# Optimization experiments

Hardware: AMD Instinct MI355X
Metric: run time of the kernel (lower is better)

## Reference

```python
import jax, jax.numpy as jnp
import numpy as np

N_ITERS = 5
STRICT_MAXIMA_BONUS = 10.0
MAX_SUBPIXEL_SHIFT = 0.6
DILATION_RADIUS = 1
EPS = 1e-7


def _dense_solve(x):
    """Per-voxel 3x3x3 quadratic-fit solve (Cramer's rule) on interior voxels.

    Returns full-size (zero-padded) sx, sy, ss, g.s, solved arrays.
    Axis convention: s = depth/scale (D), y = height (H), x = width (W).
    """
    c  = x[:, :, 1:-1, 1:-1, 1:-1]
    xp = x[:, :, 1:-1, 1:-1, 2:];   xm = x[:, :, 1:-1, 1:-1, :-2]
    yp = x[:, :, 1:-1, 2:, 1:-1];   ym = x[:, :, 1:-1, :-2, 1:-1]
    sp = x[:, :, 2:, 1:-1, 1:-1];   sm = x[:, :, :-2, 1:-1, 1:-1]
    xpyp = x[:, :, 1:-1, 2:, 2:];   xmyp = x[:, :, 1:-1, 2:, :-2]
    xpym = x[:, :, 1:-1, :-2, 2:];  xmym = x[:, :, 1:-1, :-2, :-2]
    xpsp = x[:, :, 2:, 1:-1, 2:];   xmsp = x[:, :, 2:, 1:-1, :-2]
    xpsm = x[:, :, :-2, 1:-1, 2:];  xmsm = x[:, :, :-2, 1:-1, :-2]
    ypsp = x[:, :, 2:, 2:, 1:-1];   ymsp = x[:, :, 2:, :-2, 1:-1]
    ypsm = x[:, :, :-2, 2:, 1:-1];  ymsm = x[:, :, :-2, :-2, 1:-1]
    gx = 0.5 * (xp - xm)
    gy = 0.5 * (yp - ym)
    gs = 0.5 * (sp - sm)
    dxx = xp - 2.0 * c + xm
    dyy = yp - 2.0 * c + ym
    dss = sp - 2.0 * c + sm
    dxy = 0.25 * (xpyp - xmyp - xpym + xmym)
    dxs = 0.25 * (xpsp - xmsp - xpsm + xmsm)
    dys = 0.25 * (ypsp - ymsp - ypsm + ymsm)
    cf00 = dyy * dss - dys * dys
    cf01 = dxy * dss - dys * dxs
    cf02 = dxy * dys - dyy * dxs
    det = dxx * cf00 - dxy * cf01 + dxs * cf02
    solved = jnp.abs(det) > EPS
    safe_det = jnp.where(solved, det, jnp.ones_like(det))
    r0, r1, r2 = -gx, -gy, -gs
    sx = (r0 * cf00 - dxy * (r1 * dss - dys * r2) + dxs * (r1 * dys - dyy * r2)) / safe_det
    sy = (dxx * (r1 * dss - dys * r2) - r0 * cf01 + dxs * (dxy * r2 - r1 * dxs)) / safe_det
    ss = (dxx * (dyy * r2 - r1 * dys) - dxy * (dxy * r2 - r1 * dxs) + r0 * cf02) / safe_det
    gds = gx * sx + gy * sy + gs * ss
    pad = ((0, 0), (0, 0), (1, 1), (1, 1), (1, 1))
    return (jnp.pad(sx, pad), jnp.pad(sy, pad), jnp.pad(ss, pad),
            jnp.pad(gds, pad), jnp.pad(solved, pad))


def reference(input, nms_mask):
    x = input
    B, C, D, H, W = x.shape
    dt = x.dtype
    HW = H * W
    DHW = D * HW
    r = DILATION_RADIUS

    sx_f, sy_f, ss_f, gds_f, sol_f = _dense_solve(x)
    sx_f = sx_f.reshape(-1); sy_f = sy_f.reshape(-1); ss_f = ss_f.reshape(-1)
    gds_f = gds_f.reshape(-1); sol_f = sol_f.reshape(-1)
    xf = x.reshape(-1)

    dg = jnp.arange(D, dtype=jnp.int32)[:, None, None]
    hg = jnp.arange(H, dtype=jnp.int32)[None, :, None]
    wg = jnp.arange(W, dtype=jnp.int32)[None, None, :]
    bcg = (jnp.arange(B * C, dtype=jnp.int32) * DHW).reshape(B, C, 1, 1, 1)

    zi = jnp.zeros((B, C, D, H, W), jnp.int32)
    dd, dh, dw = zi, zi, zi              # integer centre offsets (s, y, x)
    valid = nms_mask                      # only NMS maxima are tracked
    zf = jnp.zeros((B, C, D, H, W), dt)
    shift_x, shift_y, shift_s, gds_k = zf, zf, zf, zf

    for _ in range(N_ITERS):
        di = jnp.clip(dg + dd, 1, D - 2)
        hi = jnp.clip(hg + dh, 1, H - 2)
        wi = jnp.clip(wg + dw, 1, W - 2)
        flat = bcg + di * HW + hi * W + wi
        sx = sx_f[flat]; sy = sy_f[flat]; ss = ss_f[flat]
        gds = gds_f[flat]; sol = sol_f[flat]
        valid = valid & sol
        vf = valid.astype(dt)
        shift_x = sx * vf
        shift_y = sy * vf
        shift_s = ss * vf
        gds_k = gds * vf
        step_x = (jnp.sign(shift_x) * (jnp.abs(shift_x) > MAX_SUBPIXEL_SHIFT)).astype(jnp.int32)
        step_y = (jnp.sign(shift_y) * (jnp.abs(shift_y) > MAX_SUBPIXEL_SHIFT)).astype(jnp.int32)
        step_s = (jnp.sign(shift_s) * (jnp.abs(shift_s) > MAX_SUBPIXEL_SHIFT)).astype(jnp.int32)
        dw = dw + step_x; dh = dh + step_y; dd = dd + step_s
        # moving outside the dilated precompute region invalidates the keypoint
        valid = valid & (jnp.abs(dd) <= r) & (jnp.abs(dh) <= r) & (jnp.abs(dw) <= r)

    di = jnp.clip(dg + dd, 1, D - 2)
    hi = jnp.clip(hg + dh, 1, H - 2)
    wi = jnp.clip(wg + dw, 1, W - 2)
    flat = bcg + di * HW + hi * W + wi
    cur_val = xf[flat]

    refined = jnp.where(valid, cur_val + 0.5 * gds_k, x)
    y_max = jnp.where(nms_mask, refined + STRICT_MAXIMA_BONUS, x)

    fd = dg.astype(dt); fh = hg.astype(dt); fw = wg.astype(dt)
    cs = jnp.where(valid, (dg + dd).astype(dt) + shift_s, jnp.broadcast_to(fd, x.shape))
    cx = jnp.where(valid, (wg + dw).astype(dt) + shift_x, jnp.broadcast_to(fw, x.shape))
    cy = jnp.where(valid, (hg + dh).astype(dt) + shift_y, jnp.broadcast_to(fh, x.shape))
    coords_max = jnp.stack([cs, cx, cy], axis=2)  # (B,C,3,D,H,W): [scale, x, y]
    return coords_max, y_max


def setup_inputs() -> dict:
    key = jax.random.key(0)
    k1, k2 = jax.random.split(key)
    B, C, D, H, W = 2, 4, 6, 512, 512
    x = jax.random.normal(k1, (B, C, D, H, W), dtype=jnp.float32)
    m = jax.random.uniform(k2, (B, C, D, H, W)) < 0.001
    interior = jnp.zeros((B, C, D, H, W), dtype=bool).at[:, :, 1:-1, 1:-1, 1:-1].set(True)
    return {"input": x, "nms_mask": m & interior}
```

## Files before the change

### kernel.cpp

```cpp
#include <hip/hip_runtime.h>

#pragma clang fp contract(off)

constexpr int B_ = 2, C_ = 4, D_ = 6, H_ = 512, W_ = 512;
constexpr int HW_  = H_ * W_;
constexpr int DHW_ = D_ * HW_;
constexpr int BC_  = B_ * C_;
constexpr int TOT_ = BC_ * DHW_;

#define EPS_ 1e-7f
#define MAX_SHIFT_ 0.6f
#define BONUS_ 10.0f
#define N_ITERS_ 5

__device__ __forceinline__ void solve3(const float* __restrict__ p,
                                       float& sx, float& sy, float& ss,
                                       float& gds, bool& sol)
{
    #pragma clang fp contract(off)
    float c    = p[0];
    float xp   = p[1],          xm   = p[-1];
    float yp   = p[W_],         ym   = p[-W_];
    float spv  = p[HW_],        smv  = p[-HW_];
    float xpyp = p[W_ + 1],     xmyp = p[W_ - 1];
    float xpym = p[-W_ + 1],    xmym = p[-W_ - 1];
    float xpsp = p[HW_ + 1],    xmsp = p[HW_ - 1];
    float xpsm = p[-HW_ + 1],   xmsm = p[-HW_ - 1];
    float ypsp = p[HW_ + W_],   ymsp = p[HW_ - W_];
    float ypsm = p[-HW_ + W_],  ymsm = p[-HW_ - W_];

    float gx = 0.5f * (xp - xm);
    float gy = 0.5f * (yp - ym);
    float gs = 0.5f * (spv - smv);
    float dxx = xp - 2.0f * c + xm;
    float dyy = yp - 2.0f * c + ym;
    float dss = spv - 2.0f * c + smv;
    float dxy = 0.25f * (xpyp - xmyp - xpym + xmym);
    float dxs = 0.25f * (xpsp - xmsp - xpsm + xmsm);
    float dys = 0.25f * (ypsp - ymsp - ypsm + ymsm);

    float cf00 = dyy * dss - dys * dys;
    float cf01 = dxy * dss - dys * dxs;
    float cf02 = dxy * dys - dyy * dxs;
    float det  = dxx * cf00 - dxy * cf01 + dxs * cf02;
    sol = fabsf(det) > EPS_;
    float sd = sol ? det : 1.0f;
    float r0 = -gx, r1 = -gy, r2 = -gs;
    sx = (r0 * cf00 - dxy * (r1 * dss - dys * r2) + dxs * (r1 * dys - dyy * r2)) / sd;
    sy = (dxx * (r1 * dss - dys * r2) - r0 * cf01 + dxs * (dxy * r2 - r1 * dxs)) / sd;
    ss = (dxx * (dyy * r2 - r1 * dys) - dxy * (dxy * r2 - r1 * dxs) + r0 * cf02) / sd;
    gds = gx * sx + gy * sy + gs * ss;
}

__global__ __launch_bounds__(256)
void AdaptiveQuadInterp3d_kernel(const float* __restrict__ x,
                                 const int* __restrict__ mask,
                                 float* __restrict__ out)
{
    #pragma clang fp contract(off)
    int idx = blockIdx.x * 256 + threadIdx.x;
    if (idx >= TOT_) return;

    int w  = idx & (W_ - 1);
    int h  = (idx >> 9) & (H_ - 1);
    int t  = idx >> 18;
    int d  = t % D_;
    int bc = t / D_;
    int sp = idx - bc * DHW_;

    float xc = x[idx];
    bool  m  = mask[idx] != 0;

    float yv, cs, cx, cy;

    if (!m) {
        yv = xc;
        cs = (float)d;
        cx = (float)w;
        cy = (float)h;
    } else {
        const float* xb = x + bc * DHW_;
        int dd = 0, dh = 0, dwo = 0;
        bool valid = true;
        float shx = 0.0f, shy = 0.0f, shs = 0.0f, gk = 0.0f;

        #pragma unroll 1
        for (int it = 0; it < N_ITERS_; ++it) {
            int di = min(max(d + dd, 1), D_ - 2);
            int hi = min(max(h + dh, 1), H_ - 2);
            int wi = min(max(w + dwo, 1), W_ - 2);
            const float* p = xb + di * HW_ + hi * W_ + wi;

            float sx, sy, ssv, gds; bool sol;
            solve3(p, sx, sy, ssv, gds, sol);

            valid = valid && sol;
            float vf = valid ? 1.0f : 0.0f;
            shx = sx * vf;
            shy = sy * vf;
            shs = ssv * vf;
            gk  = gds * vf;

            int stx = (shx > MAX_SHIFT_) ? 1 : ((shx < -MAX_SHIFT_) ? -1 : 0);
            int sty = (shy > MAX_SHIFT_) ? 1 : ((shy < -MAX_SHIFT_) ? -1 : 0);
            int sts = (shs > MAX_SHIFT_) ? 1 : ((shs < -MAX_SHIFT_) ? -1 : 0);
            dwo += stx;
            dh  += sty;
            dd  += sts;
            valid = valid && (abs(dd) <= 1) && (abs(dh) <= 1) && (abs(dwo) <= 1);
        }

        int di = min(max(d + dd, 1), D_ - 2);
        int hi = min(max(h + dh, 1), H_ - 2);
        int wi = min(max(w + dwo, 1), W_ - 2);
        float cur = xb[di * HW_ + hi * W_ + wi];

        float refined = valid ? (cur + 0.5f * gk) : xc;
        yv = refined + BONUS_;
        cs = valid ? ((float)(d + dd) + shs) : (float)d;
        cx = valid ? ((float)(w + dwo) + shx) : (float)w;
        cy = valid ? ((float)(h + dh) + shy) : (float)h;
    }

    out[(bc * 3 + 0) * DHW_ + sp] = cs;
    out[(bc * 3 + 1) * DHW_ + sp] = cx;
    out[(bc * 3 + 2) * DHW_ + sp] = cy;
    out[BC_ * 3 * DHW_ + idx]     = yv;
}

extern "C" void kernel_launch(void* const* d_in, const int* in_sizes, int n_in,
                              void* d_out, int out_size, void* d_ws, size_t ws_size,
                              hipStream_t stream) {
    const float* x    = (const float*)d_in[0];
    const int*   mask = (const int*)d_in[1];
    float*       out  = (float*)d_out;

    int blocks = (TOT_ + 255) / 256;
    AdaptiveQuadInterp3d_kernel<<<blocks, 256, 0, stream>>>(x, mask, out);
}
```

Before: 272.5 us.

## Split into vectorized streaming pass plus sparse bitmap-driven refinement pass

Replaces the single per-voxel kernel with two passes. The first streams x and the mask as float4/int4, writes the default outputs with vector stores, and records a per-wave ballot bitmap of mask bits in workspace. The second reads that bitmap and runs the iterative quadratic refinement only for masked voxels, overwriting their outputs. This targets the memory-bound dense path and the divergent refinement inside it, at the cost of an extra launch, workspace traffic, and a fallback path when the workspace is too small.

Result: slower. 302.2 us (+10.9%).

```diff
diff --git a/kernel.cpp b/kernel.cpp
--- a/kernel.cpp
+++ b/kernel.cpp
@@ -7,6 +7,8 @@
 constexpr int DHW_ = D_ * HW_;
 constexpr int BC_  = B_ * C_;
 constexpr int TOT_ = BC_ * DHW_;
+constexpr int NWAVES_ = TOT_ / 256;
+constexpr size_t BITMAP_BYTES_ = (size_t)NWAVES_ * 4 * 8;
 
 #define EPS_ 1e-7f
 #define MAX_SHIFT_ 0.6f
@@ -52,80 +54,148 @@
     gds = gx * sx + gy * sy + gs * ss;
 }
 
-__global__ __launch_bounds__(256)
-void AdaptiveQuadInterp3d_kernel(const float* __restrict__ x,
-                                 const int* __restrict__ mask,
-                                 float* __restrict__ out)
+__device__ __forceinline__ void walk_and_write(const float* __restrict__ x,
+                                               float* __restrict__ out, int idx)
 {
     #pragma clang fp contract(off)
-    int idx = blockIdx.x * 256 + threadIdx.x;
-    if (idx >= TOT_) return;
-
     int w  = idx & (W_ - 1);
     int h  = (idx >> 9) & (H_ - 1);
     int t  = idx >> 18;
     int d  = t % D_;
     int bc = t / D_;
     int sp = idx - bc * DHW_;
-
+    const float* xb = x + bc * DHW_;
     float xc = x[idx];
-    bool  m  = mask[idx] != 0;
-
-    float yv, cs, cx, cy;
-
-    if (!m) {
-        yv = xc;
-        cs = (float)d;
-        cx = (float)w;
-        cy = (float)h;
-    } else {
-        const float* xb = x + bc * DHW_;
-        int dd = 0, dh = 0, dwo = 0;
-        bool valid = true;
-        float shx = 0.0f, shy = 0.0f, shs = 0.0f, gk = 0.0f;
-
-        #pragma unroll 1
-        for (int it = 0; it < N_ITERS_; ++it) {
-            int di = min(max(d + dd, 1), D_ - 2);
-            int hi = min(max(h + dh, 1), H_ - 2);
-            int wi = min(max(w + dwo, 1), W_ - 2);
-            const float* p = xb + di * HW_ + hi * W_ + wi;
-
-            float sx, sy, ssv, gds; bool sol;
-            solve3(p, sx, sy, ssv, gds, sol);
-
-            valid = valid && sol;
-            float vf = valid ? 1.0f : 0.0f;
-            shx = sx * vf;
-            shy = sy * vf;
-            shs = ssv * vf;
-            gk  = gds * vf;
-
-            int stx = (shx > MAX_SHIFT_) ? 1 : ((shx < -MAX_SHIFT_) ? -1 : 0);
-            int sty = (shy > MAX_SHIFT_) ? 1 : ((shy < -MAX_SHIFT_) ? -1 : 0);
-            int sts = (shs > MAX_SHIFT_) ? 1 : ((shs < -MAX_SHIFT_) ? -1 : 0);
-            dwo += stx;
-            dh  += sty;
-            dd  += sts;
-            valid = valid && (abs(dd) <= 1) && (abs(dh) <= 1) && (abs(dwo) <= 1);
-        }
-
+
+    int dd = 0, dh = 0, dwo = 0;
+    bool valid = true;
+    float shx = 0.0f, shy = 0.0f, shs = 0.0f, gk = 0.0f;
+
+    #pragma unroll 1
+    for (int it = 0; it < N_ITERS_; ++it) {
         int di = min(max(d + dd, 1), D_ - 2);
         int hi = min(max(h + dh, 1), H_ - 2);
         int wi = min(max(w + dwo, 1), W_ - 2);
-        float cur = xb[di * HW_ + hi * W_ + wi];
-
-        float refined = valid ? (cur + 0.5f * gk) : xc;
-        yv = refined + BONUS_;
-        cs = valid ? ((float)(d + dd) + shs) : (float)d;
-        cx = valid ? ((float)(w + dwo) + shx) : (float)w;
-        cy = valid ? ((float)(h + dh) + shy) : (float)h;
-    }
+        const float* p = xb + di * HW_ + hi * W_ + wi;
+
+        float sx, sy, ssv, gds; bool sol;
+        solve3(p, sx, sy, ssv, gds, sol);
+
+        valid = valid && sol;
+        float vf = valid ? 1.0f : 0.0f;
+        shx = sx * vf;
+        shy = sy * vf;
+        shs = ssv * vf;
+        gk  = gds * vf;
+
+        int stx = (shx > MAX_SHIFT_) ? 1 : ((shx < -MAX_SHIFT_) ? -1 : 0);
+        int sty = (shy > MAX_SHIFT_) ? 1 : ((shy < -MAX_SHIFT_) ? -1 : 0);
+        int sts = (shs > MAX_SHIFT_) ? 1 : ((shs < -MAX_SHIFT_) ? -1 : 0);
+        dwo += stx;
+        dh  += sty;
+        dd  += sts;
+        valid = valid && (abs(dd) <= 1) && (abs(dh) <= 1) && (abs(dwo) <= 1);
+    }
+
+    int di = min(max(d + dd, 1), D_ - 2);
+    int hi = min(max(h + dh, 1), H_ - 2);
+    int wi = min(max(w + dwo, 1), W_ - 2);
+    float cur = xb[di * HW_ + hi * W_ + wi];
+
+    float refined = valid ? (cur + 0.5f * gk) : xc;
+    float yv = refined + BONUS_;
+    float cs = valid ? ((float)(d + dd) + shs) : (float)d;
+    float cx = valid ? ((float)(w + dwo) + shx) : (float)w;
+    float cy = valid ? ((float)(h + dh) + shy) : (float)h;
 
     out[(bc * 3 + 0) * DHW_ + sp] = cs;
     out[(bc * 3 + 1) * DHW_ + sp] = cx;
     out[(bc * 3 + 2) * DHW_ + sp] = cy;
     out[BC_ * 3 * DHW_ + idx]     = yv;
+}
+
+__global__ __launch_bounds__(256)
+void stream_kernel(const float4* __restrict__ x4,
+                   const int4*  __restrict__ m4,
+                   float* __restrict__ out,
+                   unsigned long long* __restrict__ bitmap)
+{
+    int tid  = blockIdx.x * 256 + threadIdx.x;
+    int idx4 = tid << 2;
+
+    int w  = idx4 & (W_ - 1);
+    int h  = (idx4 >> 9) & (H_ - 1);
+    int t  = idx4 >> 18;
+    int d  = t % D_;
+    int bc = t / D_;
+    int sp = idx4 - bc * DHW_;
+
+    float4 xv = x4[tid];
+    int4   mv = m4[tid];
+
+    *(float4*)(out + BC_ * 3 * DHW_ + idx4) = xv;
+
+    float fd = (float)d, fh = (float)h;
+    float4 csv = {fd, fd, fd, fd};
+    float4 cxv = {(float)w, (float)(w + 1), (float)(w + 2), (float)(w + 3)};
+    float4 cyv = {fh, fh, fh, fh};
+    float* ob = out + (bc * 3) * DHW_ + sp;
+    *(float4*)(ob)            = csv;
+    *(float4*)(ob + DHW_)     = cxv;
+    *(float4*)(ob + 2 * DHW_) = cyv;
+
+    unsigned long long b0 = __ballot(mv.x != 0);
+    unsigned long long b1 = __ballot(mv.y != 0);
+    unsigned long long b2 = __ballot(mv.z != 0);
+    unsigned long long b3 = __ballot(mv.w != 0);
+    int g    = tid >> 6;
+    int lane = threadIdx.x & 63;
+    if (lane == 0) {
+        unsigned long long* bp = bitmap + (size_t)g * 4;
+        bp[0] = b0; bp[1] = b1; bp[2] = b2; bp[3] = b3;
+    }
+}
+
+__global__ __launch_bounds__(256)
+void sparse_kernel(const float* __restrict__ x,
+                   float* __restrict__ out,
+                   const unsigned long long* __restrict__ bitmap)
+{
+    int g    = (blockIdx.x * 256 + threadIdx.x) >> 6;
+    int lane = threadIdx.x & 63;
+
+    const unsigned long long* bp = bitmap + (size_t)g * 4;
+    unsigned long long b0 = bp[0], b1 = bp[1], b2 = bp[2], b3 = bp[3];
+    if ((b0 | b1 | b2 | b3) == 0ULL) return;
+
+    int base = g << 8;
+    if ((b0 >> lane) & 1ULL) walk_and_write(x, out, base + lane * 4 + 0);
+    if ((b1 >> lane) & 1ULL) walk_and_write(x, out, base + lane * 4 + 1);
+    if ((b2 >> lane) & 1ULL) walk_and_write(x, out, base + lane * 4 + 2);
+    if ((b3 >> lane) & 1ULL) walk_and_write(x, out, base + lane * 4 + 3);
+}
+
+__global__ __launch_bounds__(256)
+void fused_kernel(const float* __restrict__ x,
+                  const int* __restrict__ mask,
+                  float* __restrict__ out)
+{
+    int idx = blockIdx.x * 256 + threadIdx.x;
+    if (idx >= TOT_) return;
+    int w  = idx & (W_ - 1);
+    int h  = (idx >> 9) & (H_ - 1);
+    int t  = idx >> 18;
+    int d  = t % D_;
+    int bc = t / D_;
+    int sp = idx - bc * DHW_;
+    if (mask[idx] != 0) {
+        walk_and_write(x, out, idx);
+    } else {
+        out[(bc * 3 + 0) * DHW_ + sp] = (float)d;
+        out[(bc * 3 + 1) * DHW_ + sp] = (float)w;
+        out[(bc * 3 + 2) * DHW_ + sp] = (float)h;
+        out[BC_ * 3 * DHW_ + idx]     = x[idx];
+    }
 }
 
 extern "C" void kernel_launch(void* const* d_in, const int* in_sizes, int n_in,
@@ -135,6 +205,15 @@
     const int*   mask = (const int*)d_in[1];
     float*       out  = (float*)d_out;
 
-    int blocks = (TOT_ + 255) / 256;
-    AdaptiveQuadInterp3d_kernel<<<blocks, 256, 0, stream>>>(x, mask, out);
-}
+    if (ws_size >= BITMAP_BYTES_) {
+        unsigned long long* bitmap = (unsigned long long*)d_ws;
+        int blocksA = (TOT_ / 4) / 256;
+        stream_kernel<<<blocksA, 256, 0, stream>>>(
+            (const float4*)x, (const int4*)mask, out, bitmap);
+        int blocksB = (NWAVES_ * 64) / 256;
+        sparse_kernel<<<blocksB, 256, 0, stream>>>(x, out, bitmap);
+    } else {
+        int blocks = (TOT_ + 255) / 256;
+        fused_kernel<<<blocks, 256, 0, stream>>>(x, mask, out);
+    }
+}
```

## Vectorize to float4 per thread with default-write then sparse masked refinement

Applied to the files above, without the earlier changes.

Each thread now handles four consecutive voxels with float4/int4 loads and float4 stores, first writing the default outputs (y = x, coords = grid indices) for all four. It then skips the refinement path for the whole wavefront via a ballot when no lane has a masked voxel, and otherwise runs the iterative quadratic walk only for masked voxels, overwriting their outputs. This cuts load/store instruction count and makes writes wider. The cost is a second, scattered write for the rare masked voxels and more serial work per thread when a mask hit occurs.

Result: slower. 283.0 us (+3.8%).

```diff
diff --git a/kernel.cpp b/kernel.cpp
--- a/kernel.cpp
+++ b/kernel.cpp
@@ -52,80 +52,103 @@
     gds = gx * sx + gy * sy + gs * ss;
 }
 
-__global__ __launch_bounds__(256)
-void AdaptiveQuadInterp3d_kernel(const float* __restrict__ x,
-                                 const int* __restrict__ mask,
-                                 float* __restrict__ out)
+__device__ __forceinline__ void walk_and_write(const float* __restrict__ x,
+                                               float* __restrict__ out,
+                                               int idx, float xc)
 {
     #pragma clang fp contract(off)
-    int idx = blockIdx.x * 256 + threadIdx.x;
-    if (idx >= TOT_) return;
-
     int w  = idx & (W_ - 1);
     int h  = (idx >> 9) & (H_ - 1);
     int t  = idx >> 18;
     int d  = t % D_;
     int bc = t / D_;
     int sp = idx - bc * DHW_;
+    const float* xb = x + bc * DHW_;
 
-    float xc = x[idx];
-    bool  m  = mask[idx] != 0;
+    int dd = 0, dh = 0, dwo = 0;
+    bool valid = true;
+    float shx = 0.0f, shy = 0.0f, shs = 0.0f, gk = 0.0f;
 
-    float yv, cs, cx, cy;
-
-    if (!m) {
-        yv = xc;
-        cs = (float)d;
-        cx = (float)w;
-        cy = (float)h;
-    } else {
-        const float* xb = x + bc * DHW_;
-        int dd = 0, dh = 0, dwo = 0;
-        bool valid = true;
-        float shx = 0.0f, shy = 0.0f, shs = 0.0f, gk = 0.0f;
-
-        #pragma unroll 1
-        for (int it = 0; it < N_ITERS_; ++it) {
-            int di = min(max(d + dd, 1), D_ - 2);
-            int hi = min(max(h + dh, 1), H_ - 2);
-            int wi = min(max(w + dwo, 1), W_ - 2);
-            const float* p = xb + di * HW_ + hi * W_ + wi;
-
-            float sx, sy, ssv, gds; bool sol;
-            solve3(p, sx, sy, ssv, gds, sol);
-
-            valid = valid && sol;
-            float vf = valid ? 1.0f : 0.0f;
-            shx = sx * vf;
-            shy = sy * vf;
-            shs = ssv * vf;
-            gk  = gds * vf;
-
-            int stx = (shx > MAX_SHIFT_) ? 1 : ((shx < -MAX_SHIFT_) ? -1 : 0);
-            int sty = (shy > MAX_SHIFT_) ? 1 : ((shy < -MAX_SHIFT_) ? -1 : 0);
-            int sts = (shs > MAX_SHIFT_) ? 1 : ((shs < -MAX_SHIFT_) ? -1 : 0);
-            dwo += stx;
-            dh  += sty;
-            dd  += sts;
-            valid = valid && (abs(dd) <= 1) && (abs(dh) <= 1) && (abs(dwo) <= 1);
-        }
-
+    #pragma unroll 1
+    for (int it = 0; it < N_ITERS_; ++it) {
         int di = min(max(d + dd, 1), D_ - 2);
         int hi = min(max(h + dh, 1), H_ - 2);
         int wi = min(max(w + dwo, 1), W_ - 2);
-        float cur = xb[di * HW_ + hi * W_ + wi];
+        const float* p = xb + di * HW_ + hi * W_ + wi;
 
-        float refined = valid ? (cur + 0.5f * gk) : xc;
-        yv = refined + BONUS_;
-        cs = valid ? ((float)(d + dd) + shs) : (float)d;
-        cx = valid ? ((float)(w + dwo) + shx) : (float)w;
-        cy = valid ? ((float)(h + dh) + shy) : (float)h;
+        float sx, sy, ssv, gds; bool sol;
+        solve3(p, sx, sy, ssv, gds, sol);
+
+        valid = valid && sol;
+        float vf = valid ? 1.0f : 0.0f;
+        shx = sx * vf;
+        shy = sy * vf;
+        shs = ssv * vf;
+        gk  = gds * vf;
+
+        int stx = (shx > MAX_SHIFT_) ? 1 : ((shx < -MAX_SHIFT_) ? -1 : 0);
+        int sty = (shy > MAX_SHIFT_) ? 1 : ((shy < -MAX_SHIFT_) ? -1 : 0);
+        int sts = (shs > MAX_SHIFT_) ? 1 : ((shs < -MAX_SHIFT_) ? -1 : 0);
+        dwo += stx;
+        dh  += sty;
+        dd  += sts;
+        valid = valid && (abs(dd) <= 1) && (abs(dh) <= 1) && (abs(dwo) <= 1);
     }
+
+    int di = min(max(d + dd, 1), D_ - 2);
+    int hi = min(max(h + dh, 1), H_ - 2);
+    int wi = min(max(w + dwo, 1), W_ - 2);
+    float cur = xb[di * HW_ + hi * W_ + wi];
+
+    float refined = valid ? (cur + 0.5f * gk) : xc;
+    float yv = refined + BONUS_;
+    float cs = valid ? ((float)(d + dd) + shs) : (float)d;
+    float cx = valid ? ((float)(w + dwo) + shx) : (float)w;
+    float cy = valid ? ((float)(h + dh) + shy) : (float)h;
 
     out[(bc * 3 + 0) * DHW_ + sp] = cs;
     out[(bc * 3 + 1) * DHW_ + sp] = cx;
     out[(bc * 3 + 2) * DHW_ + sp] = cy;
     out[BC_ * 3 * DHW_ + idx]     = yv;
+}
+
+__global__ __launch_bounds__(256)
+void AdaptiveQuadInterp3d_kernel(const float4* __restrict__ x4,
+                                 const int4*  __restrict__ m4,
+                                 float* __restrict__ out)
+{
+    int tid  = blockIdx.x * 256 + threadIdx.x;
+    int idx4 = tid << 2;
+
+    int w  = idx4 & (W_ - 1);
+    int h  = (idx4 >> 9) & (H_ - 1);
+    int t  = idx4 >> 18;
+    int d  = t % D_;
+    int bc = t / D_;
+    int sp = idx4 - bc * DHW_;
+
+    float4 xv = x4[tid];
+    int4   mv = m4[tid];
+
+    *(float4*)(out + BC_ * 3 * DHW_ + idx4) = xv;
+
+    float fd = (float)d, fh = (float)h;
+    float4 csv = {fd, fd, fd, fd};
+    float4 cxv = {(float)w, (float)(w + 1), (float)(w + 2), (float)(w + 3)};
+    float4 cyv = {fh, fh, fh, fh};
+    float* ob = out + (bc * 3) * DHW_ + sp;
+    *(float4*)(ob)            = csv;
+    *(float4*)(ob + DHW_)     = cxv;
+    *(float4*)(ob + 2 * DHW_) = cyv;
+
+    bool any_lane = (mv.x | mv.y | mv.z | mv.w) != 0;
+    if (__ballot(any_lane) == 0ULL) return;
+
+    const float* x = (const float*)x4;
+    if (mv.x != 0) walk_and_write(x, out, idx4 + 0, xv.x);
+    if (mv.y != 0) walk_and_write(x, out, idx4 + 1, xv.y);
+    if (mv.z != 0) walk_and_write(x, out, idx4 + 2, xv.z);
+    if (mv.w != 0) walk_and_write(x, out, idx4 + 3, xv.w);
 }
 
 extern "C" void kernel_launch(void* const* d_in, const int* in_sizes, int n_in,
@@ -135,6 +158,7 @@
     const int*   mask = (const int*)d_in[1];
     float*       out  = (float*)d_out;
 
-    int blocks = (TOT_ + 255) / 256;
-    AdaptiveQuadInterp3d_kernel<<<blocks, 256, 0, stream>>>(x, mask, out);
+    int blocks = (TOT_ / 4) / 256;
+    AdaptiveQuadInterp3d_kernel<<<blocks, 256, 0, stream>>>(
+        (const float4*)x, (const int4*)mask, out);
 }
```
